# Kernel optimization log

Hardware: AMD Instinct MI355X
Metric: run time of the kernel (lower is better)

## Reference

```python
import jax, jax.numpy as jnp
import numpy as np

TOPK = 2  # top_k from __init__


def setup_inputs() -> dict:
    key = jax.random.key(0)
    k0, k1, k2, k3 = jax.random.split(key, 4)
    B, D, DFF, E = 8192, 1024, 1024, 32
    scale = 0.02
    return {
        "moe_inp": jax.random.normal(k0, (B, D), jnp.float32),
        "wg": jax.random.normal(k1, (D, E), jnp.float32) * scale,
        "bg": jnp.zeros((E,), jnp.float32),
        "w1": jax.random.normal(k2, (E, D, DFF), jnp.float32) * scale,
        "b1": jnp.zeros((E, DFF), jnp.float32),
        "w2": jax.random.normal(k3, (E, DFF, D), jnp.float32) * scale,
        "b2": jnp.zeros((E, D), jnp.float32),
    }


def reference(moe_inp, wg, bg, w1, b1, w2, b2):
    E = wg.shape[1]
    B = moe_inp.shape[0]
    # --- NaiveGate: linear -> top_k -> softmax over selected logits ---
    logits = moe_inp @ wg + bg                      # [B, E]
    top_val, gate_top_k_idx = jax.lax.top_k(logits, TOPK)  # [B, TOPK]
    gate_score = jax.nn.softmax(top_val, axis=-1)   # computed by gate; NOT applied
    # to expert outputs in pMoE's forward (combine is a plain sum), kept faithful.
    del gate_score
    # --- prepare_balance_forward: stable counting sort of token->expert slots ---
    gate_flat = gate_top_k_idx.reshape(-1)          # [B*TOPK] expert id per slot
    pos = jnp.argsort(gate_flat, stable=True)       # expert-sorted slot order
    fwd_expert_count = jnp.bincount(gate_flat, length=E).astype(jnp.int32)  # [E]
    # --- MoEReshape dispatch: gather token features into expert-contiguous rows ---
    x_disp = moe_inp[pos // TOPK]                   # [B*TOPK, D]
    eid = gate_flat[pos]                            # expert id per dispatched row
    # --- fused expert FFN: grouped GEMM per expert (variable-size batches) ---
    h = jax.lax.ragged_dot(x_disp, w1, fwd_expert_count) + b1[eid]  # [B*TOPK, DFF]
    h = jax.nn.gelu(h, approximate=False)
    y = jax.lax.ragged_dot(h, w2, fwd_expert_count) + b2[eid]       # [B*TOPK, D]
    # --- combine: view as [*, TOPK, D], sum topk dim, truncate to batch ---
    reduced = y.reshape(-1, TOPK, y.shape[-1]).sum(axis=1)          # [B, D]
    moe_outp = reduced[:B]
    return moe_outp, gate_top_k_idx
```

## Files before the change

### kernel.cpp

```cpp
#include <hip/hip_runtime.h>
#include <hip/hip_bf16.h>
#include <math.h>

#define NTOK 8192
#define DMODEL 1024
#define NEXP 32

typedef __attribute__((ext_vector_type(8))) short bf16x8;
typedef __attribute__((ext_vector_type(4))) float f32x4;

__device__ __forceinline__ unsigned int pk_bf16(float a, float b) {
  __hip_bfloat162 h = __float22bfloat162_rn(make_float2(a, b));
  union { __hip_bfloat162 h2; unsigned int u; } cv;
  cv.h2 = h;
  return cv.u;
}

__device__ __forceinline__ void gl_lds16(const unsigned short* g, unsigned short* l) {
  __builtin_amdgcn_global_load_lds(
      (const __attribute__((address_space(1))) unsigned int*)g,
      (__attribute__((address_space(3))) unsigned int*)l, 16, 0, 0);
}

__global__ __launch_bounds__(256) void convert_x(const float* __restrict__ x,
                                                 unsigned short* __restrict__ xb) {
  size_t i = (size_t)(blockIdx.x * 256 + threadIdx.x) * 8;
  float4 f0 = *reinterpret_cast<const float4*>(x + i);
  float4 f1 = *reinterpret_cast<const float4*>(x + i + 4);
  uint4 d;
  d.x = pk_bf16(f0.x, f0.y);
  d.y = pk_bf16(f0.z, f0.w);
  d.z = pk_bf16(f1.x, f1.y);
  d.w = pk_bf16(f1.z, f1.w);
  *reinterpret_cast<uint4*>(xb + i) = d;
}

__global__ __launch_bounds__(256) void transpose_cvt2(const float* __restrict__ w,
                                                      unsigned short* __restrict__ wt) {
  int bid = blockIdx.x;
  int e = bid >> 8;
  int tk = (bid >> 4) & 15;
  int tn = bid & 15;
  const float* src = w + ((size_t)e << 20) + ((size_t)(tk * 64) << 10) + tn * 64;
  unsigned short* dst = wt + ((size_t)e << 20) + ((size_t)(tn * 64) << 10) + tk * 64;
  __shared__ unsigned int Ts[64 * 32];
  int t = threadIdx.x;
  {
    int kp = t >> 3;
    int c8 = t & 7;
    const float* s0 = src + (size_t)(2 * kp) * 1024 + c8 * 8;
    float4 a0 = *reinterpret_cast<const float4*>(s0);
    float4 a1 = *reinterpret_cast<const float4*>(s0 + 4);
    float4 b0 = *reinterpret_cast<const float4*>(s0 + 1024);
    float4 b1 = *reinterpret_cast<const float4*>(s0 + 1028);
    float av[8] = {a0.x, a0.y, a0.z, a0.w, a1.x, a1.y, a1.z, a1.w};
    float bv[8] = {b0.x, b0.y, b0.z, b0.w, b1.x, b1.y, b1.z, b1.w};
#pragma unroll
    for (int i = 0; i < 8; i++) {
      int n = c8 * 8 + i;
      Ts[n * 32 + (kp ^ (n & 28))] = pk_bf16(av[i], bv[i]);
    }
  }
  __syncthreads();
  {
    int n = t >> 2;
    int kq = t & 3;
#pragma unroll
    for (int h = 0; h < 2; h++) {
      int k4 = kq + h * 4;
      int phys4 = (4 * k4) ^ (n & 28);
      uint4 d = *reinterpret_cast<const uint4*>(&Ts[n * 32 + phys4]);
      *reinterpret_cast<uint4*>(dst + (size_t)n * 1024 + k4 * 8) = d;
    }
  }
}

__global__ __launch_bounds__(256) void gate_partial(
    const float* __restrict__ x, const float* __restrict__ wg,
    float* __restrict__ partial) {
  __shared__ float Xs[256 * 20];
  int tid = threadIdx.x;
  int part = blockIdx.x >> 5;
  int tb = blockIdx.x & 31;
  int d0 = part * 128;
  float acc[32];
#pragma unroll
  for (int e = 0; e < 32; e++) acc[e] = 0.f;
  for (int ck = 0; ck < 8; ck++) {
    __syncthreads();
#pragma unroll
    for (int q = 0; q < 4; q++) {
      int li = q * 256 + tid;
      int row = li >> 2, j = li & 3;
      float4 v = *reinterpret_cast<const float4*>(
          x + (size_t)(tb * 256 + row) * DMODEL + d0 + ck * 16 + j * 4);
      *reinterpret_cast<float4*>(&Xs[row * 20 + j * 4]) = v;
    }
    __syncthreads();
#pragma unroll
    for (int d4 = 0; d4 < 4; d4++) {
      float4 xv = *reinterpret_cast<const float4*>(&Xs[tid * 20 + d4 * 4]);
      float xs[4] = {xv.x, xv.y, xv.z, xv.w};
#pragma unroll
      for (int dd = 0; dd < 4; dd++) {
        int d = d0 + ck * 16 + d4 * 4 + dd;
#pragma unroll
        for (int e = 0; e < 32; e++) acc[e] += xs[dd] * wg[d * 32 + e];
      }
    }
  }
  float* dst = partial + ((size_t)part * NTOK + tb * 256 + tid) * 32;
#pragma unroll
  for (int e = 0; e < 32; e += 4)
    *reinterpret_cast<float4*>(dst + e) =
        make_float4(acc[e], acc[e + 1], acc[e + 2], acc[e + 3]);
}

__global__ __launch_bounds__(256) void gate_top2(
    const float* __restrict__ partial, const float* __restrict__ bg,
    float* __restrict__ idx_out, int* __restrict__ eid,
    int* __restrict__ counts) {
  int t = blockIdx.x * 256 + threadIdx.x;
  float l[32];
#pragma unroll
  for (int e = 0; e < 32; e++) l[e] = bg[e];
  for (int p = 0; p < 8; p++) {
    const float* src = partial + ((size_t)p * NTOK + t) * 32;
#pragma unroll
    for (int e = 0; e < 32; e += 4) {
      float4 v = *reinterpret_cast<const float4*>(src + e);
      l[e] += v.x; l[e + 1] += v.y; l[e + 2] += v.z; l[e + 3] += v.w;
    }
  }
  int i0 = 0; float v0 = l[0];
#pragma unroll
  for (int e = 1; e < 32; e++)
    if (l[e] > v0) { v0 = l[e]; i0 = e; }
  int i1 = -1; float v1 = -3.0e38f;
#pragma unroll
  for (int e = 0; e < 32; e++)
    if (e != i0 && l[e] > v1) { v1 = l[e]; i1 = e; }
  *reinterpret_cast<float2*>(idx_out + t * 2) = make_float2((float)i0, (float)i1);
  eid[t * 2] = i0;
  eid[t * 2 + 1] = i1;
  atomicAdd(&counts[i0], 1);
  atomicAdd(&counts[i1], 1);
}

__global__ void scan_k(const int* __restrict__ counts, int* __restrict__ offsets) {
  if (threadIdx.x == 0) {
    int s = 0;
    for (int e = 0; e < 32; e++) { offsets[e] = s; s += counts[e]; }
    offsets[32] = s;
  }
}

__global__ __launch_bounds__(256) void build_stable(
    const int* __restrict__ eid, const int* __restrict__ offsets,
    int* __restrict__ tok_list) {
  int e = blockIdx.x;
  int tid = threadIdx.x;
  int lane = tid & 63, wv = tid >> 6;
  __shared__ int wcnt[4];
  int base = offsets[e];
  for (int c = 0; c < 64; c++) {
    int s = c * 256 + tid;
    bool f = (eid[s] == e);
    unsigned long long m = __ballot(f);
    if (lane == 0) wcnt[wv] = __popcll(m);
    __syncthreads();
    int woff = 0;
#pragma unroll
    for (int i = 0; i < 4; i++) woff += (i < wv) ? wcnt[i] : 0;
    int tot = wcnt[0] + wcnt[1] + wcnt[2] + wcnt[3];
    if (f) {
      int rank = woff + __popcll(m & ((1ull << lane) - 1ull));
      tok_list[base + rank] = s >> 1;
    }
    base += tot;
    __syncthreads();
  }
}

template <int PHASE>
__global__ __launch_bounds__(512, 2) void moe_gemm3(
    const unsigned short* __restrict__ Wt, const float* __restrict__ bias,
    const unsigned short* __restrict__ Ain, unsigned short* __restrict__ Hout,
    float* __restrict__ out, const int* __restrict__ tok_list,
    const int* __restrict__ offsets, const int* __restrict__ counts) {
  int bx = blockIdx.x;
  int e = bx & 31;
  int mt = (bx >> 5) & 3;
  int nt = (bx >> 7) & 3;
  int n_e = counts[e];
  int m0 = mt * 256;
  if (m0 >= n_e) return;
  int n0 = nt * 256;
  int seg = offsets[e];

  __shared__ __align__(16) unsigned short As[2][256 * 32];
  __shared__ __align__(16) unsigned short Bs[2][256 * 32];

  int tid = threadIdx.x, lane = tid & 63, wid = tid >> 6;
  int wm = (wid >> 2) * 128, wn = (wid & 3) * 64;
  int ml = lane & 15, q = lane >> 4;

  size_t a_off[2], b_off[2];
#pragma unroll
  for (int j = 0; j < 2; j++) {
    int arow = wid * 32 + j * 16 + (lane >> 2);
    int agr = m0 + arow;
    int acr = (agr < n_e) ? agr : (n_e - 1);
    int atok = (PHASE == 0) ? tok_list[seg + acr] : (seg + acr);
    int chunk = (lane & 3) ^ ((arow >> 1) & 3);
    a_off[j] = (size_t)atok * DMODEL + chunk * 8;
    b_off[j] = ((size_t)e * DMODEL + n0 + arow) * DMODEL + chunk * 8;
  }

  f32x4 acc[8][4];
#pragma unroll
  for (int im = 0; im < 8; im++)
#pragma unroll
    for (int in = 0; in < 4; in++) acc[im][in] = (f32x4){0.f, 0.f, 0.f, 0.f};

#define STAGE(BUF, K0)                                                  \
  {                                                                     \
    gl_lds16(Ain + a_off[0] + (K0), &As[BUF][(wid * 32) * 32]);         \
    gl_lds16(Ain + a_off[1] + (K0), &As[BUF][(wid * 32 + 16) * 32]);    \
    gl_lds16(Wt + b_off[0] + (K0), &Bs[BUF][(wid * 32) * 32]);          \
    gl_lds16(Wt + b_off[1] + (K0), &Bs[BUF][(wid * 32 + 16) * 32]);     \
  }

  STAGE(0, 0)
  STAGE(1, 32)

  for (int kt = 0; kt < 32; kt++) {
    int buf = kt & 1;
    if (kt < 31)
      asm volatile("s_waitcnt vmcnt(4)" ::: "memory");
    else
      asm volatile("s_waitcnt vmcnt(0)" ::: "memory");
    __builtin_amdgcn_s_barrier();

    bf16x8 bfr[4], af[4];
#pragma unroll
    for (int in = 0; in < 4; in++) {
      int r = wn + in * 16 + ml;
      bfr[in] = *reinterpret_cast<const bf16x8*>(
          &Bs[buf][r * 32 + ((q ^ ((r >> 1) & 3)) * 8)]);
    }
#pragma unroll
    for (int im = 0; im < 4; im++) {
      int r = wm + im * 16 + ml;
      af[im] = *reinterpret_cast<const bf16x8*>(
          &As[buf][r * 32 + ((q ^ ((r >> 1) & 3)) * 8)]);
    }
    asm volatile("s_waitcnt lgkmcnt(0)" ::: "memory");
    __builtin_amdgcn_sched_barrier(0);
    __builtin_amdgcn_s_setprio(1);
#pragma unroll
    for (int im = 0; im < 4; im++)
#pragma unroll
      for (int in = 0; in < 4; in++)
        acc[im][in] = __builtin_amdgcn_mfma_f32_16x16x32_bf16(
            af[im], bfr[in], acc[im][in], 0, 0, 0);
    __builtin_amdgcn_s_setprio(0);

    bf16x8 ag[4];
#pragma unroll
    for (int im = 0; im < 4; im++) {
      int r = wm + 64 + im * 16 + ml;
      ag[im] = *reinterpret_cast<const bf16x8*>(
          &As[buf][r * 32 + ((q ^ ((r >> 1) & 3)) * 8)]);
    }
    asm volatile("s_waitcnt lgkmcnt(0)" ::: "memory");
    __builtin_amdgcn_sched_barrier(0);
    __builtin_amdgcn_s_setprio(1);
#pragma unroll
    for (int im = 0; im < 4; im++)
#pragma unroll
      for (int in = 0; in < 4; in++)
        acc[im + 4][in] = __builtin_amdgcn_mfma_f32_16x16x32_bf16(
            ag[im], bfr[in], acc[im + 4][in], 0, 0, 0);
    __builtin_amdgcn_s_setprio(0);

    __builtin_amdgcn_s_barrier();
    if (kt < 30) {
      int k0 = (kt + 2) * 32;
      STAGE(buf, k0)
    }
  }
#undef STAGE

#pragma unroll
  for (int in = 0; in < 4; in++) {
    int n = n0 + wn + in * 16 + ml;
    float bv = bias[e * DMODEL + n];
#pragma unroll
    for (int im = 0; im < 8; im++) {
      int mb = m0 + wm + im * 16 + q * 4;
      if (PHASE == 0) {
#pragma unroll
        for (int r = 0; r < 4; r++) {
          int gr = mb + r;
          if (gr < n_e) {
            float v = acc[im][in][r] + bv;
            float g = 0.5f * v * (1.f + erff(v * 0.70710678118654752f));
            Hout[(size_t)(seg + gr) * DMODEL + n] =
                (unsigned short)(__hip_bfloat16_raw(__float2bfloat16(g)).x);
          }
        }
      } else {
        float v[4];
        bool ok[4];
#pragma unroll
        for (int r = 0; r < 4; r++) {
          ok[r] = (mb + r) < n_e;
          v[r] = acc[im][in][r] + bv;
        }
        int dp0 = seg + mb;
        if ((seg & 1) == 0) {
#pragma unroll
          for (int r = 0; r < 4; r += 2) {
            if (ok[r] && ok[r + 1])
              atomicAdd(out + (size_t)((dp0 + r) >> 1) * DMODEL + n,
                        v[r] + v[r + 1]);
            else {
              if (ok[r]) atomicAdd(out + (size_t)((dp0 + r) >> 1) * DMODEL + n, v[r]);
              if (ok[r + 1])
                atomicAdd(out + (size_t)((dp0 + r + 1) >> 1) * DMODEL + n, v[r + 1]);
            }
          }
        } else {
          if (ok[0]) atomicAdd(out + (size_t)(dp0 >> 1) * DMODEL + n, v[0]);
          if (ok[1] && ok[2])
            atomicAdd(out + (size_t)((dp0 + 1) >> 1) * DMODEL + n, v[1] + v[2]);
          else {
            if (ok[1]) atomicAdd(out + (size_t)((dp0 + 1) >> 1) * DMODEL + n, v[1]);
            if (ok[2]) atomicAdd(out + (size_t)((dp0 + 2) >> 1) * DMODEL + n, v[2]);
          }
          if (ok[3]) atomicAdd(out + (size_t)((dp0 + 3) >> 1) * DMODEL + n, v[3]);
        }
      }
    }
  }
}

extern "C" void kernel_launch(void* const* d_in, const int* in_sizes, int n_in,
                              void* d_out, int out_size, void* d_ws,
                              size_t ws_size, hipStream_t stream) {
  const float* x  = (const float*)d_in[0];
  const float* wg = (const float*)d_in[1];
  const float* bg = (const float*)d_in[2];
  const float* w1 = (const float*)d_in[3];
  const float* b1 = (const float*)d_in[4];
  const float* w2 = (const float*)d_in[5];
  const float* b2 = (const float*)d_in[6];
  float* out = (float*)d_out;

  char* w = (char*)d_ws;
  int* counts   = (int*)(w);
  int* offsets  = (int*)(w + 256);
  int* eid      = (int*)(w + 512);
  int* tok_list = (int*)(w + 512 + 65536);
  float* partial = (float*)(w + 131584);
  unsigned short* Hbuf = (unsigned short*)(w + 131584 + 8388608);
  unsigned short* Xb   = (unsigned short*)(w + 131584 + 8388608 + 33554432);
  unsigned short* w1t  = (unsigned short*)(w + 131584 + 8388608 + 33554432 + 16777216);
  unsigned short* w2t  = (unsigned short*)(w + 131584 + 8388608 + 33554432 + 16777216 + 67108864);

  hipMemsetAsync(d_ws, 0, 512, stream);
  hipMemsetAsync(d_out, 0, (size_t)NTOK * DMODEL * sizeof(float), stream);

  convert_x<<<dim3(4096), 256, 0, stream>>>(x, Xb);
  transpose_cvt2<<<dim3(8192), 256, 0, stream>>>(w1, w1t);
  transpose_cvt2<<<dim3(8192), 256, 0, stream>>>(w2, w2t);

  gate_partial<<<dim3(256), 256, 0, stream>>>(x, wg, partial);
  gate_top2<<<dim3(32), 256, 0, stream>>>(partial, bg, out + (size_t)NTOK * DMODEL,
                                          eid, counts);
  scan_k<<<1, 64, 0, stream>>>(counts, offsets);
  build_stable<<<dim3(32), 256, 0, stream>>>(eid, offsets, tok_list);

  moe_gemm3<0><<<dim3(512), 512, 0, stream>>>(w1t, b1, Xb, Hbuf, nullptr,
                                              tok_list, offsets, counts);
  moe_gemm3<1><<<dim3(512), 512, 0, stream>>>(w2t, b2, Hbuf, nullptr, out,
                                              tok_list, offsets, counts);
}
```

Before: 697.0 us.

## Shrink GEMM M-tile to 128 with 4 waves and triple-buffered LDS pipeline

Changes the grouped expert GEMM from 256x256 tiles with 8 waves to 128x256 tiles with 4 waves, so each wave covers all 128 rows over a 64-column slice. The grid doubles to 1024 blocks, which cuts wasted work on partly filled M tiles for experts with uneven token counts. LDS goes from double to triple buffering, and the next stage is issued right after the barrier instead of after compute, which removes the second barrier per k-step and overlaps loads with MFMA. In exchange, B tiles are reused across fewer rows, so weight traffic per output goes up, and LDS use per block changes.

```diff
diff --git a/kernel.cpp b/kernel.cpp
--- a/kernel.cpp
+++ b/kernel.cpp
@@ -183,29 +183,29 @@
 }
 
 template <int PHASE>
-__global__ __launch_bounds__(512, 2) void moe_gemm3(
+__global__ __launch_bounds__(256, 2) void moe_gemm3(
     const unsigned short* __restrict__ Wt, const float* __restrict__ bias,
     const unsigned short* __restrict__ Ain, unsigned short* __restrict__ Hout,
     float* __restrict__ out, const int* __restrict__ tok_list,
     const int* __restrict__ offsets, const int* __restrict__ counts) {
   int bx = blockIdx.x;
   int e = bx & 31;
-  int mt = (bx >> 5) & 3;
-  int nt = (bx >> 7) & 3;
+  int mt = (bx >> 5) & 7;
+  int nt = bx >> 8;
   int n_e = counts[e];
-  int m0 = mt * 256;
+  int m0 = mt * 128;
   if (m0 >= n_e) return;
   int n0 = nt * 256;
   int seg = offsets[e];
 
-  __shared__ __align__(16) unsigned short As[2][256 * 32];
-  __shared__ __align__(16) unsigned short Bs[2][256 * 32];
+  __shared__ __align__(16) unsigned short As[3][128 * 32];
+  __shared__ __align__(16) unsigned short Bs[3][256 * 32];
 
   int tid = threadIdx.x, lane = tid & 63, wid = tid >> 6;
-  int wm = (wid >> 2) * 128, wn = (wid & 3) * 64;
+  int wn = wid * 64;
   int ml = lane & 15, q = lane >> 4;
 
-  size_t a_off[2], b_off[2];
+  size_t a_off[2], b_off[4];
 #pragma unroll
   for (int j = 0; j < 2; j++) {
     int arow = wid * 32 + j * 16 + (lane >> 2);
@@ -214,7 +214,12 @@
     int atok = (PHASE == 0) ? tok_list[seg + acr] : (seg + acr);
     int chunk = (lane & 3) ^ ((arow >> 1) & 3);
     a_off[j] = (size_t)atok * DMODEL + chunk * 8;
-    b_off[j] = ((size_t)e * DMODEL + n0 + arow) * DMODEL + chunk * 8;
+  }
+#pragma unroll
+  for (int p = 0; p < 4; p++) {
+    int brow = wid * 64 + p * 16 + (lane >> 2);
+    int chunk = (lane & 3) ^ ((brow >> 1) & 3);
+    b_off[p] = ((size_t)e * DMODEL + n0 + brow) * DMODEL + chunk * 8;
   }
 
   f32x4 acc[8][4];
@@ -227,22 +232,30 @@
   {                                                                     \
     gl_lds16(Ain + a_off[0] + (K0), &As[BUF][(wid * 32) * 32]);         \
     gl_lds16(Ain + a_off[1] + (K0), &As[BUF][(wid * 32 + 16) * 32]);    \
-    gl_lds16(Wt + b_off[0] + (K0), &Bs[BUF][(wid * 32) * 32]);          \
-    gl_lds16(Wt + b_off[1] + (K0), &Bs[BUF][(wid * 32 + 16) * 32]);     \
+    gl_lds16(Wt + b_off[0] + (K0), &Bs[BUF][(wid * 64) * 32]);          \
+    gl_lds16(Wt + b_off[1] + (K0), &Bs[BUF][(wid * 64 + 16) * 32]);     \
+    gl_lds16(Wt + b_off[2] + (K0), &Bs[BUF][(wid * 64 + 32) * 32]);     \
+    gl_lds16(Wt + b_off[3] + (K0), &Bs[BUF][(wid * 64 + 48) * 32]);     \
   }
 
   STAGE(0, 0)
   STAGE(1, 32)
 
   for (int kt = 0; kt < 32; kt++) {
-    int buf = kt & 1;
+    int buf = kt - (kt / 3) * 3;
     if (kt < 31)
-      asm volatile("s_waitcnt vmcnt(4)" ::: "memory");
+      asm volatile("s_waitcnt vmcnt(6)" ::: "memory");
     else
       asm volatile("s_waitcnt vmcnt(0)" ::: "memory");
     __builtin_amdgcn_s_barrier();
-
-    bf16x8 bfr[4], af[4];
+    if (kt < 30) {
+      int nb = kt + 2;
+      int buf2 = nb - (nb / 3) * 3;
+      int k0 = nb * 32;
+      STAGE(buf2, k0)
+    }
+
+    bf16x8 bfr[4], af[8];
 #pragma unroll
     for (int in = 0; in < 4; in++) {
       int r = wn + in * 16 + ml;
@@ -250,8 +263,8 @@
           &Bs[buf][r * 32 + ((q ^ ((r >> 1) & 3)) * 8)]);
     }
 #pragma unroll
-    for (int im = 0; im < 4; im++) {
-      int r = wm + im * 16 + ml;
+    for (int im = 0; im < 8; im++) {
+      int r = im * 16 + ml;
       af[im] = *reinterpret_cast<const bf16x8*>(
           &As[buf][r * 32 + ((q ^ ((r >> 1) & 3)) * 8)]);
     }
@@ -259,36 +272,12 @@
     __builtin_amdgcn_sched_barrier(0);
     __builtin_amdgcn_s_setprio(1);
 #pragma unroll
-    for (int im = 0; im < 4; im++)
+    for (int im = 0; im < 8; im++)
 #pragma unroll
       for (int in = 0; in < 4; in++)
         acc[im][in] = __builtin_amdgcn_mfma_f32_16x16x32_bf16(
             af[im], bfr[in], acc[im][in], 0, 0, 0);
     __builtin_amdgcn_s_setprio(0);
-
-    bf16x8 ag[4];
-#pragma unroll
-    for (int im = 0; im < 4; im++) {
-      int r = wm + 64 + im * 16 + ml;
-      ag[im] = *reinterpret_cast<const bf16x8*>(
-          &As[buf][r * 32 + ((q ^ ((r >> 1) & 3)) * 8)]);
-    }
-    asm volatile("s_waitcnt lgkmcnt(0)" ::: "memory");
-    __builtin_amdgcn_sched_barrier(0);
-    __builtin_amdgcn_s_setprio(1);
-#pragma unroll
-    for (int im = 0; im < 4; im++)
-#pragma unroll
-      for (int in = 0; in < 4; in++)
-        acc[im + 4][in] = __builtin_amdgcn_mfma_f32_16x16x32_bf16(
-            ag[im], bfr[in], acc[im + 4][in], 0, 0, 0);
-    __builtin_amdgcn_s_setprio(0);
-
-    __builtin_amdgcn_s_barrier();
-    if (kt < 30) {
-      int k0 = (kt + 2) * 32;
-      STAGE(buf, k0)
-    }
   }
 #undef STAGE
 
@@ -298,7 +287,7 @@
     float bv = bias[e * DMODEL + n];
 #pragma unroll
     for (int im = 0; im < 8; im++) {
-      int mb = m0 + wm + im * 16 + q * 4;
+      int mb = m0 + im * 16 + q * 4;
       if (PHASE == 0) {
 #pragma unroll
         for (int r = 0; r < 4; r++) {
@@ -382,8 +371,8 @@
   scan_k<<<1, 64, 0, stream>>>(counts, offsets);
   build_stable<<<dim3(32), 256, 0, stream>>>(eid, offsets, tok_list);
 
-  moe_gemm3<0><<<dim3(512), 512, 0, stream>>>(w1t, b1, Xb, Hbuf, nullptr,
-                                              tok_list, offsets, counts);
-  moe_gemm3<1><<<dim3(512), 512, 0, stream>>>(w2t, b2, Hbuf, nullptr, out,
-                                              tok_list, offsets, counts);
-}
+  moe_gemm3<0><<<dim3(1024), 256, 0, stream>>>(w1t, b1, Xb, Hbuf, nullptr,
+                                               tok_list, offsets, counts);
+  moe_gemm3<1><<<dim3(1024), 256, 0, stream>>>(w2t, b2, Hbuf, nullptr, out,
+                                               tok_list, offsets, counts);
+}
```

New measurement: 666.5 us. 4.4% less time.
